# Optimization experiments

Hardware: AMD Instinct MI355X
Metric: run time of the kernel (lower is better)

## Reference

```python
import jax, jax.numpy as jnp
import numpy as np

N = 6144
HIDDEN = 48
HEADS = 3
HEAD = HIDDEN // HEADS


def setup_inputs() -> dict:
    key = jax.random.key(0)
    ks = jax.random.split(key, 8)
    s = 1.0 / np.sqrt(HIDDEN)
    A = (jax.random.uniform(ks[0], (N, N)) < 0.05).astype(jnp.float32)
    h = jax.random.normal(ks[1], (N, HIDDEN), dtype=jnp.float32)
    Wq = jax.random.normal(ks[2], (HIDDEN, HIDDEN), dtype=jnp.float32) * s
    Wk = jax.random.normal(ks[3], (HIDDEN, HIDDEN), dtype=jnp.float32) * s
    Wv = jax.random.normal(ks[4], (HIDDEN, HIDDEN), dtype=jnp.float32) * s
    bq = jnp.zeros((HIDDEN,), jnp.float32)
    bk = jnp.zeros((HIDDEN,), jnp.float32)
    bv = jnp.zeros((HIDDEN,), jnp.float32)
    return {"A": A, "h": h, "Wq": Wq, "bq": bq, "Wk": Wk, "bk": bk, "Wv": Wv, "bv": bv}


def reference(A, h, Wq, bq, Wk, bk, Wv, bv):
    n = h.shape[0]
    # QKV projections (torch Linear: x @ W.T + b)
    q = (h @ Wq.T + bq).reshape(n, HEADS, HEAD).transpose(1, 0, 2)  # [H,N,d]
    k = (h @ Wk.T + bk).reshape(n, HEADS, HEAD).transpose(1, 0, 2)
    v = (h @ Wv.T + bv).reshape(n, HEADS, HEAD).transpose(1, 0, 2)
    # scores = (q k^T) * A / N**(-0.5)  == (q k^T) * A * sqrt(N)  (faithful to source)
    scale = jnp.asarray(n, h.dtype) ** 0.5
    scores = jnp.einsum("hnd,hmd->hnm", q, k) * A[None, :, :] * scale
    scores = jax.nn.softmax(scores, axis=2)
    out = jnp.einsum("hnm,hmd->hnd", scores, v)  # [H,N,d]
    out = out.transpose(1, 0, 2).reshape(n, HIDDEN)
    return (out, scores)
```

## Files before the change

### kernel.cpp

```cpp
#include <hip/hip_runtime.h>
#include <math.h>

#define NN   6144
#define HID  48
#define BLK  512
#define RPB  4
#define CAP  448
#define CTOT (RPB*CAP)
#define NSL  42
#define SCALE 78.38367176906175f

typedef float vf4 __attribute__((ext_vector_type(4)));

__global__ __launch_bounds__(256)
void qkv_kernel(const float* __restrict__ h,
                const float* __restrict__ Wq, const float* __restrict__ bq,
                const float* __restrict__ Wk, const float* __restrict__ bk,
                const float* __restrict__ Wv, const float* __restrict__ bv,
                float* __restrict__ qw, float* __restrict__ kw, float* __restrict__ vw) {
    int idx = blockIdx.x * blockDim.x + threadIdx.x;
    int i = idx / HID, c = idx % HID;
    const float4* h4  = (const float4*)(h + (size_t)i * HID);
    const float4* wq4 = (const float4*)(Wq + (size_t)c * HID);
    const float4* wk4 = (const float4*)(Wk + (size_t)c * HID);
    const float4* wv4 = (const float4*)(Wv + (size_t)c * HID);
    float aq = 0.f, ak = 0.f, av = 0.f;
    #pragma unroll
    for (int r = 0; r < HID / 4; ++r) {
        float4 hv = h4[r];
        float4 q4 = wq4[r], k4 = wk4[r], v4 = wv4[r];
        aq = fmaf(hv.x, q4.x, aq); aq = fmaf(hv.y, q4.y, aq);
        aq = fmaf(hv.z, q4.z, aq); aq = fmaf(hv.w, q4.w, aq);
        ak = fmaf(hv.x, k4.x, ak); ak = fmaf(hv.y, k4.y, ak);
        ak = fmaf(hv.z, k4.z, ak); ak = fmaf(hv.w, k4.w, ak);
        av = fmaf(hv.x, v4.x, av); av = fmaf(hv.y, v4.y, av);
        av = fmaf(hv.z, v4.z, av); av = fmaf(hv.w, v4.w, av);
    }
    aq += bq[c]; ak += bk[c]; av += bv[c];
    int head = c >> 4, d = c & 15;
    size_t off = ((size_t)head * NN + i) * 16 + d;
    qw[off] = aq; kw[off] = ak; vw[off] = av;
}

__global__ __launch_bounds__(256)
void vtot_kernel(const float* __restrict__ vw, float* __restrict__ vtot) {
    int c = blockIdx.x;
    int head = c >> 4, d = c & 15;
    float s = 0.f;
    for (int j = threadIdx.x; j < NN; j += 256)
        s += vw[((size_t)head * NN + j) * 16 + d];
    #pragma unroll
    for (int o = 32; o; o >>= 1) s += __shfl_xor(s, o, 64);
    __shared__ float red[4];
    int wid = threadIdx.x >> 6, lane = threadIdx.x & 63;
    if (lane == 0) red[wid] = s;
    __syncthreads();
    if (threadIdx.x == 0) vtot[c] = red[0] + red[1] + red[2] + red[3];
}

__device__ __forceinline__ float maxw(const float* w, int idx) {
    float m = 0.f;
    #pragma unroll
    for (int k = 0; k < 8; ++k) m = fmaxf(m, w[k * 12 + idx]);
    return m;
}
__device__ __forceinline__ float sumw(const float* w, int idx) {
    float s = 0.f;
    #pragma unroll
    for (int k = 0; k < 8; ++k) s += w[k * 12 + idx];
    return s;
}

__global__ __launch_bounds__(BLK)
void attn_kernel(const float* __restrict__ A,
                 const float* __restrict__ qw, const float* __restrict__ kw,
                 const float* __restrict__ vw, const float* __restrict__ vtot,
                 float* __restrict__ out) {
    __shared__ int   list[CTOT];
    __shared__ float sc[3][CTOT];
    __shared__ __align__(16) float qs[RPB * 48];
    __shared__ float accL[RPB * 52];
    __shared__ float wredM[8 * 12];
    __shared__ float wredL[8 * 12];
    __shared__ unsigned wlo[8], whi[8];

    const int i0 = blockIdx.x * RPB;
    const int tid = threadIdx.x;
    const int wid = tid >> 6, lane = tid & 63;

    if (tid < RPB * 48) {
        int r = tid / 48, c = tid % 48;
        int hh = c >> 4, d = c & 15;
        qs[tid] = qw[((size_t)hh * NN + (i0 + r)) * 16 + d];
    }
    if (tid < RPB * 52) accL[tid] = 0.f;

    unsigned long long amask = 0ull;
    #pragma unroll
    for (int r = 0; r < RPB; ++r) {
        const vf4* Ar = (const vf4*)(A + (size_t)(i0 + r) * NN);
        #pragma unroll
        for (int c = 0; c < 3; ++c) {
            vf4 a4 = __builtin_nontemporal_load(&Ar[tid + c * BLK]);
            int p = r * 16 + c * 4;
            if (a4.x != 0.f) amask |= 1ull << (p + 0);
            if (a4.y != 0.f) amask |= 1ull << (p + 1);
            if (a4.z != 0.f) amask |= 1ull << (p + 2);
            if (a4.w != 0.f) amask |= 1ull << (p + 3);
        }
    }
    unsigned m0 = (unsigned)(amask & 0xFFFull);
    unsigned m1 = (unsigned)((amask >> 16) & 0xFFFull);
    unsigned m2 = (unsigned)((amask >> 32) & 0xFFFull);
    unsigned m3 = (unsigned)((amask >> 48) & 0xFFFull);
    unsigned lo = (unsigned)__popc(m0) | ((unsigned)__popc(m1) << 16);
    unsigned hi = (unsigned)__popc(m2) | ((unsigned)__popc(m3) << 16);

    unsigned ilo = lo, ihi = hi;
    #pragma unroll
    for (int o = 1; o < 64; o <<= 1) {
        unsigned plo = __shfl_up(ilo, o, 64);
        unsigned phi = __shfl_up(ihi, o, 64);
        if (lane >= o) { ilo += plo; ihi += phi; }
    }
    if (lane == 63) { wlo[wid] = ilo; whi[wid] = ihi; }
    __syncthreads();
    unsigned blo = ilo - lo, bhi = ihi - hi;
    unsigned tlo = 0, thi = 0;
    #pragma unroll
    for (int w = 0; w < 8; ++w) {
        unsigned a = wlo[w], b = whi[w];
        if (w < wid) { blo += a; bhi += b; }
        tlo += a; thi += b;
    }
    const int C0 = min((int)(tlo & 0xFFFFu), CAP), C1 = min((int)(tlo >> 16), CAP);
    const int C2 = min((int)(thi & 0xFFFFu), CAP), C3 = min((int)(thi >> 16), CAP);
    const int cum1 = C0, cum2 = C0 + C1, cum3 = cum2 + C2;
    const int Ctot = cum3 + C3;
    int bs[4] = {(int)(blo & 0xFFFFu), (int)(blo >> 16),
                 (int)(bhi & 0xFFFFu), (int)(bhi >> 16)};
    int cu[5] = {0, cum1, cum2, cum3, Ctot};
    unsigned mr[4] = {m0, m1, m2, m3};
    int Cr4[4] = {C0, C1, C2, C3};

    #pragma unroll
    for (int r = 0; r < RPB; ++r) {
        unsigned m = mr[r];
        int b = bs[r];
        while (m) {
            int p = __ffs(m) - 1; m &= m - 1;
            if (b < CAP) list[cu[r] + b] = 4 * (tid + (p >> 2) * BLK) + (p & 3);
            ++b;
        }
    }
    __syncthreads();

    float mx[3][4];
    #pragma unroll
    for (int hh = 0; hh < 3; ++hh)
        #pragma unroll
        for (int r = 0; r < 4; ++r) mx[hh][r] = 0.f;
    {
        const int part = tid & 3;
        #pragma unroll
        for (int hh = 0; hh < 3; ++hh) {
            for (int e = (tid >> 2); e < Ctot; e += (BLK >> 2)) {
                int r = (e >= cum1) + (e >= cum2) + (e >= cum3);
                int j = list[e];
                float4 kv = ((const float4*)(kw + ((size_t)hh * NN + j) * 16))[part];
                float4 qv = ((const float4*)(qs + r * 48 + hh * 16))[part];
                float d = qv.x * kv.x;
                d = fmaf(qv.y, kv.y, d);
                d = fmaf(qv.z, kv.z, d);
                d = fmaf(qv.w, kv.w, d);
                d += __shfl_xor(d, 1, 64);
                d += __shfl_xor(d, 2, 64);
                float s = d * SCALE;
                if (part == 0) sc[hh][e] = s;
                mx[hh][0] = (r == 0) ? fmaxf(mx[hh][0], s) : mx[hh][0];
                mx[hh][1] = (r == 1) ? fmaxf(mx[hh][1], s) : mx[hh][1];
                mx[hh][2] = (r == 2) ? fmaxf(mx[hh][2], s) : mx[hh][2];
                mx[hh][3] = (r == 3) ? fmaxf(mx[hh][3], s) : mx[hh][3];
            }
        }
    }
    #pragma unroll
    for (int o = 32; o; o >>= 1)
        #pragma unroll
        for (int hh = 0; hh < 3; ++hh)
            #pragma unroll
            for (int r = 0; r < 4; ++r)
                mx[hh][r] = fmaxf(mx[hh][r], __shfl_xor(mx[hh][r], o, 64));
    if (lane == 0) {
        #pragma unroll
        for (int r = 0; r < 4; ++r)
            #pragma unroll
            for (int hh = 0; hh < 3; ++hh) wredM[wid * 12 + r * 3 + hh] = mx[hh][r];
    }
    __syncthreads();

    #pragma unroll
    for (int r = 0; r < RPB; ++r) {
        float M0 = maxw(wredM, r * 3 + 0);
        float M1 = maxw(wredM, r * 3 + 1);
        float M2 = maxw(wredM, r * 3 + 2);
        float l0 = 0.f, l1 = 0.f, l2 = 0.f;
        for (int e = cu[r] + tid; e < cu[r + 1]; e += BLK) {
            float p0 = __expf(sc[0][e] - M0); sc[0][e] = p0; l0 += p0;
            float p1 = __expf(sc[1][e] - M1); sc[1][e] = p1; l1 += p1;
            float p2 = __expf(sc[2][e] - M2); sc[2][e] = p2; l2 += p2;
        }
        #pragma unroll
        for (int o = 32; o; o >>= 1) {
            l0 += __shfl_xor(l0, o, 64);
            l1 += __shfl_xor(l1, o, 64);
            l2 += __shfl_xor(l2, o, 64);
        }
        if (lane == 0) {
            wredL[wid * 12 + r * 3 + 0] = l0;
            wredL[wid * 12 + r * 3 + 1] = l1;
            wredL[wid * 12 + r * 3 + 2] = l2;
        }
    }
    __syncthreads();

    float* Pp = out + (size_t)NN * HID;

    #pragma unroll
    for (int r = 0; r < RPB; ++r) {
        float M0 = maxw(wredM, r * 3 + 0), M1 = maxw(wredM, r * 3 + 1), M2 = maxw(wredM, r * 3 + 2);
        float z0 = __expf(-M0), z1 = __expf(-M1), z2 = __expf(-M2);
        float fc = (float)(NN - Cr4[r]);
        float iv0 = 1.0f / (sumw(wredL, r * 3 + 0) + fc * z0);
        float iv1 = 1.0f / (sumw(wredL, r * 3 + 1) + fc * z1);
        float iv2 = 1.0f / (sumw(wredL, r * 3 + 2) + fc * z2);
        float zi0 = z0 * iv0, zi1 = z1 * iv1, zi2 = z2 * iv2;
        int b = bs[r];
        unsigned m = mr[r];
        size_t rowoff = (size_t)(i0 + r) * NN;
        #pragma unroll
        for (int c = 0; c < 3; ++c) {
            vf4 P0, P1, P2;
            #pragma unroll
            for (int e = 0; e < 4; ++e) {
                int p = c * 4 + e;
                bool nz = (m >> p) & 1u;
                if (nz && b < CAP) {
                    int slot = cu[r] + b;
                    P0[e] = sc[0][slot] * iv0;
                    P1[e] = sc[1][slot] * iv1;
                    P2[e] = sc[2][slot] * iv2;
                } else {
                    P0[e] = zi0; P1[e] = zi1; P2[e] = zi2;
                }
                b += nz ? 1 : 0;
            }
            __builtin_nontemporal_store(P0, &((vf4*)(Pp + 0 * (size_t)NN * NN + rowoff))[tid + c * BLK]);
            __builtin_nontemporal_store(P1, &((vf4*)(Pp + 1 * (size_t)NN * NN + rowoff))[tid + c * BLK]);
            __builtin_nontemporal_store(P2, &((vf4*)(Pp + 2 * (size_t)NN * NN + rowoff))[tid + c * BLK]);
        }
    }

    if (tid < NSL * 12) {
        int s = tid % 12, a = tid / 12;
        int hh = s >> 2, rr4 = s & 3;
        const float* vbase = vw + (size_t)hh * NN * 16 + rr4 * 4;
        #pragma unroll
        for (int r = 0; r < RPB; ++r) {
            float zz = __expf(-maxw(wredM, r * 3 + hh));
            float ax = 0.f, ay = 0.f, az = 0.f, aw = 0.f;
            #pragma unroll 2
            for (int e = cu[r] + a; e < cu[r + 1]; e += NSL) {
                int j = list[e];
                float w = sc[hh][e] - zz;
                float4 vv = *(const float4*)(vbase + (size_t)j * 16);
                ax = fmaf(w, vv.x, ax);
                ay = fmaf(w, vv.y, ay);
                az = fmaf(w, vv.z, az);
                aw = fmaf(w, vv.w, aw);
            }
            int cb = r * 52 + hh * 16 + rr4 * 4;
            atomicAdd(&accL[cb + 0], ax);
            atomicAdd(&accL[cb + 1], ay);
            atomicAdd(&accL[cb + 2], az);
            atomicAdd(&accL[cb + 3], aw);
        }
    }
    __syncthreads();

    if (tid < RPB * 48) {
        int r = tid / 48, c = tid % 48, hh = c >> 4;
        float M = maxw(wredM, r * 3 + hh);
        float z = __expf(-M);
        float iv = 1.0f / (sumw(wredL, r * 3 + hh) + (float)(NN - Cr4[r]) * z);
        out[(size_t)(i0 + r) * HID + c] = (accL[r * 52 + c] + z * vtot[c]) * iv;
    }
}

extern "C" void kernel_launch(void* const* d_in, const int* in_sizes, int n_in,
                              void* d_out, int out_size, void* d_ws, size_t ws_size,
                              hipStream_t stream) {
    const float* A  = (const float*)d_in[0];
    const float* h  = (const float*)d_in[1];
    const float* Wq = (const float*)d_in[2];
    const float* bq = (const float*)d_in[3];
    const float* Wk = (const float*)d_in[4];
    const float* bk = (const float*)d_in[5];
    const float* Wv = (const float*)d_in[6];
    const float* bv = (const float*)d_in[7];
    float* out = (float*)d_out;
    float* ws  = (float*)d_ws;

    float* qw   = ws;
    float* kw   = ws + (size_t)3 * NN * 16;
    float* vw   = ws + (size_t)6 * NN * 16;
    float* vtot = ws + (size_t)9 * NN * 16;

    qkv_kernel<<<(NN * HID) / 256, 256, 0, stream>>>(h, Wq, bq, Wk, bk, Wv, bv, qw, kw, vw);
    vtot_kernel<<<HID, 256, 0, stream>>>(vw, vtot);
    attn_kernel<<<NN / RPB, BLK, 0, stream>>>(A, qw, kw, vw, vtot, out);
}
```

Measured before the change: 635.9 us.

## Split probability write into separate fill-and-scatter kernel, halve rows per block

```diff
diff --git a/kernel.cpp b/kernel.cpp
--- a/kernel.cpp
+++ b/kernel.cpp
@@ -3,11 +3,11 @@
 
 #define NN   6144
 #define HID  48
-#define BLK  512
-#define RPB  4
+#define BLK  256
+#define RPB  2
 #define CAP  448
 #define CTOT (RPB*CAP)
-#define NSL  42
+#define NSL  21
 #define SCALE 78.38367176906175f
 
 typedef float vf4 __attribute__((ext_vector_type(4)));
@@ -58,31 +58,33 @@
     if (threadIdx.x == 0) vtot[c] = red[0] + red[1] + red[2] + red[3];
 }
 
-__device__ __forceinline__ float maxw(const float* w, int idx) {
+__device__ __forceinline__ float maxw4(const float* w, int idx) {
     float m = 0.f;
     #pragma unroll
-    for (int k = 0; k < 8; ++k) m = fmaxf(m, w[k * 12 + idx]);
+    for (int k = 0; k < 4; ++k) m = fmaxf(m, w[k * 6 + idx]);
     return m;
 }
-__device__ __forceinline__ float sumw(const float* w, int idx) {
+__device__ __forceinline__ float sumw4(const float* w, int idx) {
     float s = 0.f;
     #pragma unroll
-    for (int k = 0; k < 8; ++k) s += w[k * 12 + idx];
+    for (int k = 0; k < 4; ++k) s += w[k * 6 + idx];
     return s;
 }
 
 __global__ __launch_bounds__(BLK)
-void attn_kernel(const float* __restrict__ A,
-                 const float* __restrict__ qw, const float* __restrict__ kw,
-                 const float* __restrict__ vw, const float* __restrict__ vtot,
-                 float* __restrict__ out) {
+void attn_compute(const float* __restrict__ A,
+                  const float* __restrict__ qw, const float* __restrict__ kw,
+                  const float* __restrict__ vw, const float* __restrict__ vtot,
+                  float* __restrict__ out,
+                  float* __restrict__ zinvg, int* __restrict__ cntg,
+                  vf4* __restrict__ pwg, int* __restrict__ listg) {
     __shared__ int   list[CTOT];
     __shared__ float sc[3][CTOT];
     __shared__ __align__(16) float qs[RPB * 48];
     __shared__ float accL[RPB * 52];
-    __shared__ float wredM[8 * 12];
-    __shared__ float wredL[8 * 12];
-    __shared__ unsigned wlo[8], whi[8];
+    __shared__ float wredM[4 * 6];
+    __shared__ float wredL[4 * 6];
+    __shared__ unsigned wcnt[4];
 
     const int i0 = blockIdx.x * RPB;
     const int tid = threadIdx.x;
@@ -95,53 +97,46 @@
     }
     if (tid < RPB * 52) accL[tid] = 0.f;
 
-    unsigned long long amask = 0ull;
+    unsigned mr[RPB];
     #pragma unroll
     for (int r = 0; r < RPB; ++r) {
         const vf4* Ar = (const vf4*)(A + (size_t)(i0 + r) * NN);
-        #pragma unroll
-        for (int c = 0; c < 3; ++c) {
+        unsigned m = 0;
+        #pragma unroll
+        for (int c = 0; c < 6; ++c) {
             vf4 a4 = __builtin_nontemporal_load(&Ar[tid + c * BLK]);
-            int p = r * 16 + c * 4;
-            if (a4.x != 0.f) amask |= 1ull << (p + 0);
-            if (a4.y != 0.f) amask |= 1ull << (p + 1);
-            if (a4.z != 0.f) amask |= 1ull << (p + 2);
-            if (a4.w != 0.f) amask |= 1ull << (p + 3);
-        }
-    }
-    unsigned m0 = (unsigned)(amask & 0xFFFull);
-    unsigned m1 = (unsigned)((amask >> 16) & 0xFFFull);
-    unsigned m2 = (unsigned)((amask >> 32) & 0xFFFull);
-    unsigned m3 = (unsigned)((amask >> 48) & 0xFFFull);
-    unsigned lo = (unsigned)__popc(m0) | ((unsigned)__popc(m1) << 16);
-    unsigned hi = (unsigned)__popc(m2) | ((unsigned)__popc(m3) << 16);
-
-    unsigned ilo = lo, ihi = hi;
+            int p = c * 4;
+            if (a4.x != 0.f) m |= 1u << (p + 0);
+            if (a4.y != 0.f) m |= 1u << (p + 1);
+            if (a4.z != 0.f) m |= 1u << (p + 2);
+            if (a4.w != 0.f) m |= 1u << (p + 3);
+        }
+        mr[r] = m;
+    }
+    unsigned lo = (unsigned)__popc(mr[0]) | ((unsigned)__popc(mr[1]) << 16);
+
+    unsigned ilo = lo;
     #pragma unroll
     for (int o = 1; o < 64; o <<= 1) {
-        unsigned plo = __shfl_up(ilo, o, 64);
-        unsigned phi = __shfl_up(ihi, o, 64);
-        if (lane >= o) { ilo += plo; ihi += phi; }
-    }
-    if (lane == 63) { wlo[wid] = ilo; whi[wid] = ihi; }
-    __syncthreads();
-    unsigned blo = ilo - lo, bhi = ihi - hi;
-    unsigned tlo = 0, thi = 0;
-    #pragma unroll
-    for (int w = 0; w < 8; ++w) {
-        unsigned a = wlo[w], b = whi[w];
-        if (w < wid) { blo += a; bhi += b; }
-        tlo += a; thi += b;
-    }
-    const int C0 = min((int)(tlo & 0xFFFFu), CAP), C1 = min((int)(tlo >> 16), CAP);
-    const int C2 = min((int)(thi & 0xFFFFu), CAP), C3 = min((int)(thi >> 16), CAP);
-    const int cum1 = C0, cum2 = C0 + C1, cum3 = cum2 + C2;
-    const int Ctot = cum3 + C3;
-    int bs[4] = {(int)(blo & 0xFFFFu), (int)(blo >> 16),
-                 (int)(bhi & 0xFFFFu), (int)(bhi >> 16)};
-    int cu[5] = {0, cum1, cum2, cum3, Ctot};
-    unsigned mr[4] = {m0, m1, m2, m3};
-    int Cr4[4] = {C0, C1, C2, C3};
+        unsigned p = __shfl_up(ilo, o, 64);
+        if (lane >= o) ilo += p;
+    }
+    if (lane == 63) wcnt[wid] = ilo;
+    __syncthreads();
+    unsigned blo = ilo - lo;
+    unsigned tlo = 0;
+    #pragma unroll
+    for (int w = 0; w < 4; ++w) {
+        unsigned a = wcnt[w];
+        if (w < wid) blo += a;
+        tlo += a;
+    }
+    const int C0 = min((int)(tlo & 0xFFFFu), CAP);
+    const int C1 = min((int)(tlo >> 16), CAP);
+    const int cum1 = C0, Ctot = C0 + C1;
+    int bs[RPB] = {(int)(blo & 0xFFFFu), (int)(blo >> 16)};
+    int cu[RPB + 1] = {0, cum1, Ctot};
+    int Cr4[RPB] = {C0, C1};
 
     #pragma unroll
     for (int r = 0; r < RPB; ++r) {
@@ -155,17 +150,17 @@
     }
     __syncthreads();
 
-    float mx[3][4];
+    float mx[3][RPB];
     #pragma unroll
     for (int hh = 0; hh < 3; ++hh)
         #pragma unroll
-        for (int r = 0; r < 4; ++r) mx[hh][r] = 0.f;
+        for (int r = 0; r < RPB; ++r) mx[hh][r] = 0.f;
     {
         const int part = tid & 3;
         #pragma unroll
         for (int hh = 0; hh < 3; ++hh) {
             for (int e = (tid >> 2); e < Ctot; e += (BLK >> 2)) {
-                int r = (e >= cum1) + (e >= cum2) + (e >= cum3);
+                int r = (e >= cum1);
                 int j = list[e];
                 float4 kv = ((const float4*)(kw + ((size_t)hh * NN + j) * 16))[part];
                 float4 qv = ((const float4*)(qs + r * 48 + hh * 16))[part];
@@ -179,8 +174,6 @@
                 if (part == 0) sc[hh][e] = s;
                 mx[hh][0] = (r == 0) ? fmaxf(mx[hh][0], s) : mx[hh][0];
                 mx[hh][1] = (r == 1) ? fmaxf(mx[hh][1], s) : mx[hh][1];
-                mx[hh][2] = (r == 2) ? fmaxf(mx[hh][2], s) : mx[hh][2];
-                mx[hh][3] = (r == 3) ? fmaxf(mx[hh][3], s) : mx[hh][3];
             }
         }
     }
@@ -189,21 +182,21 @@
         #pragma unroll
         for (int hh = 0; hh < 3; ++hh)
             #pragma unroll
-            for (int r = 0; r < 4; ++r)
+            for (int r = 0; r < RPB; ++r)
                 mx[hh][r] = fmaxf(mx[hh][r], __shfl_xor(mx[hh][r], o, 64));
     if (lane == 0) {
         #pragma unroll
-        for (int r = 0; r < 4; ++r)
+        for (int r = 0; r < RPB; ++r)
             #pragma unroll
-            for (int hh = 0; hh < 3; ++hh) wredM[wid * 12 + r * 3 + hh] = mx[hh][r];
+            for (int hh = 0; hh < 3; ++hh) wredM[wid * 6 + r * 3 + hh] = mx[hh][r];
     }
     __syncthreads();
 
     #pragma unroll
     for (int r = 0; r < RPB; ++r) {
-        float M0 = maxw(wredM, r * 3 + 0);
-        float M1 = maxw(wredM, r * 3 + 1);
-        float M2 = maxw(wredM, r * 3 + 2);
+        float M0 = maxw4(wredM, r * 3 + 0);
+        float M1 = maxw4(wredM, r * 3 + 1);
+        float M2 = maxw4(wredM, r * 3 + 2);
         float l0 = 0.f, l1 = 0.f, l2 = 0.f;
         for (int e = cu[r] + tid; e < cu[r + 1]; e += BLK) {
             float p0 = __expf(sc[0][e] - M0); sc[0][e] = p0; l0 += p0;
@@ -217,47 +210,30 @@
             l2 += __shfl_xor(l2, o, 64);
         }
         if (lane == 0) {
-            wredL[wid * 12 + r * 3 + 0] = l0;
-            wredL[wid * 12 + r * 3 + 1] = l1;
-            wredL[wid * 12 + r * 3 + 2] = l2;
-        }
-    }
-    __syncthreads();
-
-    float* Pp = out + (size_t)NN * HID;
+            wredL[wid * 6 + r * 3 + 0] = l0;
+            wredL[wid * 6 + r * 3 + 1] = l1;
+            wredL[wid * 6 + r * 3 + 2] = l2;
+        }
+    }
+    __syncthreads();
 
     #pragma unroll
     for (int r = 0; r < RPB; ++r) {
-        float M0 = maxw(wredM, r * 3 + 0), M1 = maxw(wredM, r * 3 + 1), M2 = maxw(wredM, r * 3 + 2);
+        float M0 = maxw4(wredM, r * 3 + 0), M1 = maxw4(wredM, r * 3 + 1), M2 = maxw4(wredM, r * 3 + 2);
         float z0 = __expf(-M0), z1 = __expf(-M1), z2 = __expf(-M2);
         float fc = (float)(NN - Cr4[r]);
-        float iv0 = 1.0f / (sumw(wredL, r * 3 + 0) + fc * z0);
-        float iv1 = 1.0f / (sumw(wredL, r * 3 + 1) + fc * z1);
-        float iv2 = 1.0f / (sumw(wredL, r * 3 + 2) + fc * z2);
-        float zi0 = z0 * iv0, zi1 = z1 * iv1, zi2 = z2 * iv2;
-        int b = bs[r];
-        unsigned m = mr[r];
-        size_t rowoff = (size_t)(i0 + r) * NN;
-        #pragma unroll
-        for (int c = 0; c < 3; ++c) {
-            vf4 P0, P1, P2;
-            #pragma unroll
-            for (int e = 0; e < 4; ++e) {
-                int p = c * 4 + e;
-                bool nz = (m >> p) & 1u;
-                if (nz && b < CAP) {
-                    int slot = cu[r] + b;
-                    P0[e] = sc[0][slot] * iv0;
-                    P1[e] = sc[1][slot] * iv1;
-                    P2[e] = sc[2][slot] * iv2;
-                } else {
-                    P0[e] = zi0; P1[e] = zi1; P2[e] = zi2;
-                }
-                b += nz ? 1 : 0;
-            }
-            __builtin_nontemporal_store(P0, &((vf4*)(Pp + 0 * (size_t)NN * NN + rowoff))[tid + c * BLK]);
-            __builtin_nontemporal_store(P1, &((vf4*)(Pp + 1 * (size_t)NN * NN + rowoff))[tid + c * BLK]);
-            __builtin_nontemporal_store(P2, &((vf4*)(Pp + 2 * (size_t)NN * NN + rowoff))[tid + c * BLK]);
+        float iv0 = 1.0f / (sumw4(wredL, r * 3 + 0) + fc * z0);
+        float iv1 = 1.0f / (sumw4(wredL, r * 3 + 1) + fc * z1);
+        float iv2 = 1.0f / (sumw4(wredL, r * 3 + 2) + fc * z2);
+        if (tid == 0) {
+            ((vf4*)zinvg)[i0 + r] = (vf4){z0 * iv0, z1 * iv1, z2 * iv2, 0.f};
+            cntg[i0 + r] = Cr4[r];
+        }
+        size_t gbase = (size_t)(i0 + r) * CAP;
+        for (int e = cu[r] + tid; e < cu[r + 1]; e += BLK) {
+            int idx = e - cu[r];
+            pwg[gbase + idx] = (vf4){sc[0][e] * iv0, sc[1][e] * iv1, sc[2][e] * iv2, 0.f};
+            listg[gbase + idx] = list[e];
         }
     }
 
@@ -267,7 +243,7 @@
         const float* vbase = vw + (size_t)hh * NN * 16 + rr4 * 4;
         #pragma unroll
         for (int r = 0; r < RPB; ++r) {
-            float zz = __expf(-maxw(wredM, r * 3 + hh));
+            float zz = __expf(-maxw4(wredM, r * 3 + hh));
             float ax = 0.f, ay = 0.f, az = 0.f, aw = 0.f;
             #pragma unroll 2
             for (int e = cu[r] + a; e < cu[r + 1]; e += NSL) {
@@ -290,10 +266,42 @@
 
     if (tid < RPB * 48) {
         int r = tid / 48, c = tid % 48, hh = c >> 4;
-        float M = maxw(wredM, r * 3 + hh);
+        float M = maxw4(wredM, r * 3 + hh);
         float z = __expf(-M);
-        float iv = 1.0f / (sumw(wredL, r * 3 + hh) + (float)(NN - Cr4[r]) * z);
+        float iv = 1.0f / (sumw4(wredL, r * 3 + hh) + (float)(NN - Cr4[r]) * z);
         out[(size_t)(i0 + r) * HID + c] = (accL[r * 52 + c] + z * vtot[c]) * iv;
+    }
+}
+
+__global__ __launch_bounds__(256)
+void pwrite_kernel(const float* __restrict__ zinvg, const int* __restrict__ cntg,
+                   const vf4* __restrict__ pwg, const int* __restrict__ listg,
+                   float* __restrict__ out) {
+    const int row = blockIdx.x;
+    const int tid = threadIdx.x;
+    vf4 zf = ((const vf4*)zinvg)[row];
+    const int C = cntg[row];
+    float* P0 = out + (size_t)NN * HID + (size_t)row * NN;
+    float* P1 = P0 + (size_t)NN * NN;
+    float* P2 = P1 + (size_t)NN * NN;
+    vf4 z0v = (vf4){zf.x, zf.x, zf.x, zf.x};
+    vf4 z1v = (vf4){zf.y, zf.y, zf.y, zf.y};
+    vf4 z2v = (vf4){zf.z, zf.z, zf.z, zf.z};
+    #pragma unroll
+    for (int k = 0; k < 6; ++k) {
+        int idx = tid + k * 256;
+        ((vf4*)P0)[idx] = z0v;
+        ((vf4*)P1)[idx] = z1v;
+        ((vf4*)P2)[idx] = z2v;
+    }
+    __syncthreads();
+    size_t gbase = (size_t)row * CAP;
+    for (int e = tid; e < C; e += 256) {
+        vf4 pv = pwg[gbase + e];
+        int j = listg[gbase + e];
+        P0[j] = pv.x;
+        P1[j] = pv.y;
+        P2[j] = pv.z;
     }
 }
 
@@ -315,8 +323,14 @@
     float* kw   = ws + (size_t)3 * NN * 16;
     float* vw   = ws + (size_t)6 * NN * 16;
     float* vtot = ws + (size_t)9 * NN * 16;
+    float* zinvg = vtot + 64;
+    int*   cntg  = (int*)(zinvg + (size_t)NN * 4);
+    vf4*   pwg   = (vf4*)(cntg + NN);
+    int*   listg = (int*)(pwg + (size_t)NN * CAP);
 
     qkv_kernel<<<(NN * HID) / 256, 256, 0, stream>>>(h, Wq, bq, Wk, bk, Wv, bv, qw, kw, vw);
     vtot_kernel<<<HID, 256, 0, stream>>>(vw, vtot);
-    attn_kernel<<<NN / RPB, BLK, 0, stream>>>(A, qw, kw, vw, vtot, out);
-}
+    attn_compute<<<NN / RPB, BLK, 0, stream>>>(A, qw, kw, vw, vtot, out,
+                                               zinvg, cntg, pwg, listg);
+    pwrite_kernel<<<NN, 256, 0, stream>>>(zinvg, cntg, pwg, listg, out);
+}
```

Result: slower. 720.1 us (+13.2%).

## Fuse score max and exp-sum into online softmax, drop separate exp pass

Applied to the files above, without the earlier changes.

```diff
diff --git a/kernel.cpp b/kernel.cpp
--- a/kernel.cpp
+++ b/kernel.cpp
@@ -58,17 +58,14 @@
     if (threadIdx.x == 0) vtot[c] = red[0] + red[1] + red[2] + red[3];
 }
 
-__device__ __forceinline__ float maxw(const float* w, int idx) {
-    float m = 0.f;
-    #pragma unroll
-    for (int k = 0; k < 8; ++k) m = fmaxf(m, w[k * 12 + idx]);
-    return m;
-}
-__device__ __forceinline__ float sumw(const float* w, int idx) {
-    float s = 0.f;
-    #pragma unroll
-    for (int k = 0; k < 8; ++k) s += w[k * 12 + idx];
-    return s;
+__device__ __forceinline__ void combineML(const float* wm, const float* wl,
+                                          int idx, float& M, float& Lc) {
+    M = 0.f;
+    #pragma unroll
+    for (int k = 0; k < 8; ++k) M = fmaxf(M, wm[k * 12 + idx]);
+    Lc = 0.f;
+    #pragma unroll
+    for (int k = 0; k < 8; ++k) Lc += wl[k * 12 + idx] * __expf(wm[k * 12 + idx] - M);
 }
 
 __global__ __launch_bounds__(BLK)
@@ -136,10 +133,9 @@
     const int C0 = min((int)(tlo & 0xFFFFu), CAP), C1 = min((int)(tlo >> 16), CAP);
     const int C2 = min((int)(thi & 0xFFFFu), CAP), C3 = min((int)(thi >> 16), CAP);
     const int cum1 = C0, cum2 = C0 + C1, cum3 = cum2 + C2;
-    const int Ctot = cum3 + C3;
     int bs[4] = {(int)(blo & 0xFFFFu), (int)(blo >> 16),
                  (int)(bhi & 0xFFFFu), (int)(bhi >> 16)};
-    int cu[5] = {0, cum1, cum2, cum3, Ctot};
+    int cu[5] = {0, cum1, cum2, cum3, cum3 + C3};
     unsigned mr[4] = {m0, m1, m2, m3};
     int Cr4[4] = {C0, C1, C2, C3};
 
@@ -155,85 +151,80 @@
     }
     __syncthreads();
 
-    float mx[3][4];
-    #pragma unroll
-    for (int hh = 0; hh < 3; ++hh)
+    {
+        const int q4 = tid >> 2, part = tid & 3;
         #pragma unroll
-        for (int r = 0; r < 4; ++r) mx[hh][r] = 0.f;
-    {
-        const int part = tid & 3;
-        #pragma unroll
-        for (int hh = 0; hh < 3; ++hh) {
-            for (int e = (tid >> 2); e < Ctot; e += (BLK >> 2)) {
-                int r = (e >= cum1) + (e >= cum2) + (e >= cum3);
+        for (int r = 0; r < RPB; ++r) {
+            float4 qv0 = ((const float4*)(qs + r * 48 +  0))[part];
+            float4 qv1 = ((const float4*)(qs + r * 48 + 16))[part];
+            float4 qv2 = ((const float4*)(qs + r * 48 + 32))[part];
+            float om0 = 0.f, om1 = 0.f, om2 = 0.f;
+            float ol0 = 0.f, ol1 = 0.f, ol2 = 0.f;
+            int e0 = cu[r] + ((q4 - cu[r]) & 127);
+            for (int e = e0; e < cu[r + 1]; e += 128) {
                 int j = list[e];
-                float4 kv = ((const float4*)(kw + ((size_t)hh * NN + j) * 16))[part];
-                float4 qv = ((const float4*)(qs + r * 48 + hh * 16))[part];
-                float d = qv.x * kv.x;
-                d = fmaf(qv.y, kv.y, d);
-                d = fmaf(qv.z, kv.z, d);
-                d = fmaf(qv.w, kv.w, d);
-                d += __shfl_xor(d, 1, 64);
-                d += __shfl_xor(d, 2, 64);
-                float s = d * SCALE;
-                if (part == 0) sc[hh][e] = s;
-                mx[hh][0] = (r == 0) ? fmaxf(mx[hh][0], s) : mx[hh][0];
-                mx[hh][1] = (r == 1) ? fmaxf(mx[hh][1], s) : mx[hh][1];
-                mx[hh][2] = (r == 2) ? fmaxf(mx[hh][2], s) : mx[hh][2];
-                mx[hh][3] = (r == 3) ? fmaxf(mx[hh][3], s) : mx[hh][3];
-            }
-        }
-    }
-    #pragma unroll
-    for (int o = 32; o; o >>= 1)
-        #pragma unroll
-        for (int hh = 0; hh < 3; ++hh)
+                float4 k0 = ((const float4*)(kw + ((size_t)0 * NN + j) * 16))[part];
+                float4 k1 = ((const float4*)(kw + ((size_t)1 * NN + j) * 16))[part];
+                float4 k2 = ((const float4*)(kw + ((size_t)2 * NN + j) * 16))[part];
+                float d0 = k0.x * qv0.x; d0 = fmaf(k0.y, qv0.y, d0);
+                d0 = fmaf(k0.z, qv0.z, d0); d0 = fmaf(k0.w, qv0.w, d0);
+                float d1 = k1.x * qv1.x; d1 = fmaf(k1.y, qv1.y, d1);
+                d1 = fmaf(k1.z, qv1.z, d1); d1 = fmaf(k1.w, qv1.w, d1);
+                float d2 = k2.x * qv2.x; d2 = fmaf(k2.y, qv2.y, d2);
+                d2 = fmaf(k2.z, qv2.z, d2); d2 = fmaf(k2.w, qv2.w, d2);
+                d0 += __shfl_xor(d0, 1, 64); d0 += __shfl_xor(d0, 2, 64);
+                d1 += __shfl_xor(d1, 1, 64); d1 += __shfl_xor(d1, 2, 64);
+                d2 += __shfl_xor(d2, 1, 64); d2 += __shfl_xor(d2, 2, 64);
+                float s0 = d0 * SCALE, s1 = d1 * SCALE, s2 = d2 * SCALE;
+                if (part == 0) {
+                    sc[0][e] = s0; sc[1][e] = s1; sc[2][e] = s2;
+                    float nh, t;
+                    nh = fmaxf(om0, s0); t = __expf(fminf(om0, s0) - nh);
+                    ol0 = (s0 > om0) ? fmaf(ol0, t, 1.0f) : (ol0 + t); om0 = nh;
+                    nh = fmaxf(om1, s1); t = __expf(fminf(om1, s1) - nh);
+                    ol1 = (s1 > om1) ? fmaf(ol1, t, 1.0f) : (ol1 + t); om1 = nh;
+                    nh = fmaxf(om2, s2); t = __expf(fminf(om2, s2) - nh);
+                    ol2 = (s2 > om2) ? fmaf(ol2, t, 1.0f) : (ol2 + t); om2 = nh;
+                }
+            }
+            float M0 = om0, M1 = om1, M2 = om2;
             #pragma unroll
-            for (int r = 0; r < 4; ++r)
-                mx[hh][r] = fmaxf(mx[hh][r], __shfl_xor(mx[hh][r], o, 64));
-    if (lane == 0) {
-        #pragma unroll
-        for (int r = 0; r < 4; ++r)
+            for (int o = 32; o; o >>= 1) {
+                M0 = fmaxf(M0, __shfl_xor(M0, o, 64));
+                M1 = fmaxf(M1, __shfl_xor(M1, o, 64));
+                M2 = fmaxf(M2, __shfl_xor(M2, o, 64));
+            }
+            float L0 = ol0 * __expf(om0 - M0);
+            float L1 = ol1 * __expf(om1 - M1);
+            float L2 = ol2 * __expf(om2 - M2);
             #pragma unroll
-            for (int hh = 0; hh < 3; ++hh) wredM[wid * 12 + r * 3 + hh] = mx[hh][r];
-    }
-    __syncthreads();
+            for (int o = 32; o; o >>= 1) {
+                L0 += __shfl_xor(L0, o, 64);
+                L1 += __shfl_xor(L1, o, 64);
+                L2 += __shfl_xor(L2, o, 64);
+            }
+            if (lane == 0) {
+                wredM[wid * 12 + r * 3 + 0] = M0; wredL[wid * 12 + r * 3 + 0] = L0;
+                wredM[wid * 12 + r * 3 + 1] = M1; wredL[wid * 12 + r * 3 + 1] = L1;
+                wredM[wid * 12 + r * 3 + 2] = M2; wredL[wid * 12 + r * 3 + 2] = L2;
+            }
+        }
+    }
+    __syncthreads();
+
+    float* Pp = out + (size_t)NN * HID;
 
     #pragma unroll
     for (int r = 0; r < RPB; ++r) {
-        float M0 = maxw(wredM, r * 3 + 0);
-        float M1 = maxw(wredM, r * 3 + 1);
-        float M2 = maxw(wredM, r * 3 + 2);
-        float l0 = 0.f, l1 = 0.f, l2 = 0.f;
-        for (int e = cu[r] + tid; e < cu[r + 1]; e += BLK) {
-            float p0 = __expf(sc[0][e] - M0); sc[0][e] = p0; l0 += p0;
-            float p1 = __expf(sc[1][e] - M1); sc[1][e] = p1; l1 += p1;
-            float p2 = __expf(sc[2][e] - M2); sc[2][e] = p2; l2 += p2;
-        }
-        #pragma unroll
-        for (int o = 32; o; o >>= 1) {
-            l0 += __shfl_xor(l0, o, 64);
-            l1 += __shfl_xor(l1, o, 64);
-            l2 += __shfl_xor(l2, o, 64);
-        }
-        if (lane == 0) {
-            wredL[wid * 12 + r * 3 + 0] = l0;
-            wredL[wid * 12 + r * 3 + 1] = l1;
-            wredL[wid * 12 + r * 3 + 2] = l2;
-        }
-    }
-    __syncthreads();
-
-    float* Pp = out + (size_t)NN * HID;
-
-    #pragma unroll
-    for (int r = 0; r < RPB; ++r) {
-        float M0 = maxw(wredM, r * 3 + 0), M1 = maxw(wredM, r * 3 + 1), M2 = maxw(wredM, r * 3 + 2);
+        float M0, L0, M1, L1, M2, L2;
+        combineML(wredM, wredL, r * 3 + 0, M0, L0);
+        combineML(wredM, wredL, r * 3 + 1, M1, L1);
+        combineML(wredM, wredL, r * 3 + 2, M2, L2);
         float z0 = __expf(-M0), z1 = __expf(-M1), z2 = __expf(-M2);
         float fc = (float)(NN - Cr4[r]);
-        float iv0 = 1.0f / (sumw(wredL, r * 3 + 0) + fc * z0);
-        float iv1 = 1.0f / (sumw(wredL, r * 3 + 1) + fc * z1);
-        float iv2 = 1.0f / (sumw(wredL, r * 3 + 2) + fc * z2);
+        float iv0 = 1.0f / (L0 + fc * z0);
+        float iv1 = 1.0f / (L1 + fc * z1);
+        float iv2 = 1.0f / (L2 + fc * z2);
         float zi0 = z0 * iv0, zi1 = z1 * iv1, zi2 = z2 * iv2;
         int b = bs[r];
         unsigned m = mr[r];
@@ -247,9 +238,9 @@
                 bool nz = (m >> p) & 1u;
                 if (nz && b < CAP) {
                     int slot = cu[r] + b;
-                    P0[e] = sc[0][slot] * iv0;
-                    P1[e] = sc[1][slot] * iv1;
-                    P2[e] = sc[2][slot] * iv2;
+                    P0[e] = __expf(sc[0][slot] - M0) * iv0;
+                    P1[e] = __expf(sc[1][slot] - M1) * iv1;
+                    P2[e] = __expf(sc[2][slot] - M2) * iv2;
                 } else {
                     P0[e] = zi0; P1[e] = zi1; P2[e] = zi2;
                 }
@@ -267,12 +258,14 @@
         const float* vbase = vw + (size_t)hh * NN * 16 + rr4 * 4;
         #pragma unroll
         for (int r = 0; r < RPB; ++r) {
-            float zz = __expf(-maxw(wredM, r * 3 + hh));
+            float M, L;
+            combineML(wredM, wredL, r * 3 + hh, M, L);
+            float zz = __expf(-M);
             float ax = 0.f, ay = 0.f, az = 0.f, aw = 0.f;
             #pragma unroll 2
             for (int e = cu[r] + a; e < cu[r + 1]; e += NSL) {
                 int j = list[e];
-                float w = sc[hh][e] - zz;
+                float w = __expf(sc[hh][e] - M) - zz;
                 float4 vv = *(const float4*)(vbase + (size_t)j * 16);
                 ax = fmaf(w, vv.x, ax);
                 ay = fmaf(w, vv.y, ay);
@@ -290,9 +283,10 @@
 
     if (tid < RPB * 48) {
         int r = tid / 48, c = tid % 48, hh = c >> 4;
-        float M = maxw(wredM, r * 3 + hh);
+        float M, L;
+        combineML(wredM, wredL, r * 3 + hh, M, L);
         float z = __expf(-M);
-        float iv = 1.0f / (sumw(wredL, r * 3 + hh) + (float)(NN - Cr4[r]) * z);
+        float iv = 1.0f / (L + (float)(NN - Cr4[r]) * z);
         out[(size_t)(i0 + r) * HID + c] = (accL[r * 52 + c] + z * vtot[c]) * iv;
     }
 }
```

Measured after the change: 658.8 us. 3.6% more time.
